# Performance work log

Hardware: AMD Instinct MI355X
Metric: run time of the kernel (lower is better)

## Reference

```python
import jax, jax.numpy as jnp
import numpy as np

B, L, D, H = 2, 2048, 1024, 16
DK = D // H  # head_dim = 64


def setup_inputs() -> dict:
    key = jax.random.key(0)
    ks = jax.random.split(key, 12)
    init = lambda k, shape, fan_in: jax.random.uniform(k, shape, jnp.float32, -1.0, 1.0) / np.sqrt(fan_in)
    inp = {
        "query": jax.random.normal(ks[0], (B, L, D), jnp.float32),
        "key": jax.random.normal(ks[1], (B, L, D), jnp.float32),
        "value": jax.random.normal(ks[2], (B, L, D), jnp.float32),
        # causal mask [B, 1, L, L], True = attend
        "mask": jnp.broadcast_to(jnp.tril(jnp.ones((L, L), bool))[None, None], (B, 1, L, L)),
        "wq": init(ks[3], (D, D), D), "bq": jnp.zeros((D,), jnp.float32),
        "wk": init(ks[4], (D, D), D), "bk": jnp.zeros((D,), jnp.float32),
        "wv": init(ks[5], (D, D), D), "bv": jnp.zeros((D,), jnp.float32),
        "wo": init(ks[6], (D, D), D), "bo": jnp.zeros((D,), jnp.float32),
    }
    return inp


def reference(query, key, value, mask, wq, bq, wk, bk, wv, bv, wo, bo):
    b, l, d = query.shape
    split = lambda x: x.reshape(b, l, H, DK).transpose(0, 2, 1, 3)  # B H L dk
    Q = split(query @ wq + bq)
    K = split(key @ wk + bk)
    V = split(value @ wv + bv)
    scores = jnp.einsum("bhqd,bhkd->bhqk", Q, K) / jnp.sqrt(jnp.float32(DK))
    probs = jax.nn.softmax(scores, axis=-1, where=mask)  # masked-out rows contribute 0
    attn = jnp.einsum("bhqk,bhkd->bhqd", probs, V)
    out = attn.transpose(0, 2, 1, 3).reshape(b, l, d)  # B L D
    return out @ wo + bo
```

## Files before the change

### kernel.cpp

```cpp
#include <hip/hip_runtime.h>
#include <hip/hip_bf16.h>

typedef __bf16 bf16x8 __attribute__((ext_vector_type(8)));
typedef __bf16 bf16x4 __attribute__((ext_vector_type(4)));
typedef float floatx4 __attribute__((ext_vector_type(4)));

constexpr int Bn  = 2;
constexpr int Ln  = 2048;
constexpr int Dn  = 1024;
constexpr int Hn  = 16;
constexpr int DKn = 64;
constexpr int Mn  = Bn * Ln;

__device__ __forceinline__ void gload_lds16(const void* g, void* l) {
  __builtin_amdgcn_global_load_lds(
      (const __attribute__((address_space(1))) void*)g,
      (__attribute__((address_space(3))) void*)l, 16, 0, 0);
}

__global__ __launch_bounds__(256) void cvt3(
    const float* __restrict__ q, const float* __restrict__ k,
    const float* __restrict__ v, __hip_bfloat16* __restrict__ dst)
{
  const float* src = blockIdx.z == 0 ? q : blockIdx.z == 1 ? k : v;
  __hip_bfloat16* d = dst + (size_t)blockIdx.z * Mn * Dn;
  const int i = blockIdx.x * 256 + threadIdx.x;
  const float4 a = ((const float4*)src)[i * 2];
  const float4 b = ((const float4*)src)[i * 2 + 1];
  bf16x8 o;
  o[0] = (__bf16)a.x; o[1] = (__bf16)a.y; o[2] = (__bf16)a.z; o[3] = (__bf16)a.w;
  o[4] = (__bf16)b.x; o[5] = (__bf16)b.y; o[6] = (__bf16)b.z; o[7] = (__bf16)b.w;
  ((bf16x8*)d)[i] = o;
}

__global__ __launch_bounds__(256) void transpose4(
    const float* __restrict__ wq, const float* __restrict__ wk,
    const float* __restrict__ wv, const float* __restrict__ wo,
    __hip_bfloat16* __restrict__ out)
{
  const float* src = blockIdx.z == 0 ? wq : blockIdx.z == 1 ? wk
                   : blockIdx.z == 2 ? wv : wo;
  __hip_bfloat16* dst = out + (size_t)blockIdx.z * Dn * Dn;
  __shared__ __bf16 tile[32][33];
  const int tx = threadIdx.x, ty = threadIdx.y;
  const int x = blockIdx.x * 32 + tx;
  const int y = blockIdx.y * 32 + ty;
  for (int i = 0; i < 32; i += 8)
    tile[ty + i][tx] = (__bf16)src[(size_t)(y + i) * Dn + x];
  __syncthreads();
  const int x2 = blockIdx.y * 32 + tx;
  const int y2 = blockIdx.x * 32 + ty;
  for (int i = 0; i < 32; i += 8)
    ((__bf16*)dst)[(size_t)(y2 + i) * Dn + x2] = tile[tx][ty + i];
}

__global__ __launch_bounds__(256) void gemm_qkv(
    const __hip_bfloat16* __restrict__ Abf,
    const __hip_bfloat16* __restrict__ wT,
    const float* __restrict__ bq, const float* __restrict__ bk,
    const float* __restrict__ bv,
    __hip_bfloat16* __restrict__ Qp, __hip_bfloat16* __restrict__ Kp,
    __hip_bfloat16* __restrict__ Vt)
{
  constexpr int BK = 32;
  __shared__ __bf16 As[128][BK];
  __shared__ __bf16 Ws[128][BK];
  const int z = blockIdx.z;
  const __hip_bfloat16* A  = Abf + (size_t)z * Mn * Dn;
  const __hip_bfloat16* WT = wT  + (size_t)z * Dn * Dn;
  const float* bias = z == 0 ? bq : z == 1 ? bk : bv;

  const int m0 = blockIdx.x * 128;
  const int n0 = blockIdx.y * 128;
  const int tid  = threadIdx.x;
  const int lane = tid & 63;
  const int wave = tid >> 6;
  const int quad = lane >> 4;
  const int l16  = lane & 15;
  const int wm = (wave >> 1) * 64;
  const int wn = (wave & 1) * 64;
  const int srow = tid >> 2;
  const int scol = (tid & 3) * 8;

  floatx4 acc[4][4];
  for (int i = 0; i < 4; i++)
    for (int j = 0; j < 4; j++)
      acc[i][j] = (floatx4){0.f, 0.f, 0.f, 0.f};

  for (int k0 = 0; k0 < Dn; k0 += BK) {
    for (int half = 0; half < 2; half++) {
      gload_lds16(&A [(size_t)(m0 + srow + half * 64) * Dn + k0 + scol],
                  &As[srow + half * 64][scol]);
      gload_lds16(&WT[(size_t)(n0 + srow + half * 64) * Dn + k0 + scol],
                  &Ws[srow + half * 64][scol]);
    }
    __syncthreads();
    bf16x8 af[4], wf[4];
    for (int i = 0; i < 4; i++) af[i] = *(const bf16x8*)&As[wm + i * 16 + l16][quad * 8];
    for (int j = 0; j < 4; j++) wf[j] = *(const bf16x8*)&Ws[wn + j * 16 + l16][quad * 8];
    for (int i = 0; i < 4; i++)
      for (int j = 0; j < 4; j++)
        acc[i][j] = __builtin_amdgcn_mfma_f32_16x16x32_bf16(af[i], wf[j], acc[i][j], 0, 0, 0);
    __syncthreads();
  }

  if (z == 2) {
    for (int j = 0; j < 4; j++) {
      const int n = n0 + wn + j * 16 + l16;
      const float bvv = bias[n];
      const int h = n >> 6, dk = n & 63;
      for (int i = 0; i < 4; i++) {
        const int m = m0 + wm + i * 16 + quad * 4;
        const int b = m >> 11, li = m & (Ln - 1);
        bf16x4 pk;
        for (int r = 0; r < 4; r++) pk[r] = (__bf16)(acc[i][j][r] + bvv);
        *(bf16x4*)&Vt[(((size_t)(b * Hn + h)) * DKn + dk) * Ln + li] = pk;
      }
    }
  } else {
    __hip_bfloat16* out = z == 0 ? Qp : Kp;
    for (int j = 0; j < 4; j++) {
      const int n = n0 + wn + j * 16 + l16;
      const float bvv = bias[n];
      const int h = n >> 6, dk = n & 63;
      for (int i = 0; i < 4; i++) {
        for (int r = 0; r < 4; r++) {
          const int m = m0 + wm + i * 16 + quad * 4 + r;
          const int b = m >> 11, li = m & (Ln - 1);
          out[(((size_t)(b * Hn + h)) * Ln + li) * DKn + dk] =
              __float2bfloat16(acc[i][j][r] + bvv);
        }
      }
    }
  }
}

__global__ __launch_bounds__(256) void gemm_out(
    const __hip_bfloat16* __restrict__ A,
    const __hip_bfloat16* __restrict__ WT,
    const float* __restrict__ bias,
    float* __restrict__ out)
{
  constexpr int BK = 32;
  __shared__ __bf16 As[128][BK];
  __shared__ __bf16 Ws[64][BK];
  const int m0 = blockIdx.x * 128;
  const int n0 = blockIdx.y * 64;
  const int tid  = threadIdx.x;
  const int lane = tid & 63;
  const int wave = tid >> 6;
  const int quad = lane >> 4;
  const int l16  = lane & 15;
  const int wm = (wave >> 1) * 64;
  const int wn = (wave & 1) * 32;
  const int srow = tid >> 2;
  const int scol = (tid & 3) * 8;

  floatx4 acc[4][2];
  for (int i = 0; i < 4; i++)
    for (int j = 0; j < 2; j++)
      acc[i][j] = (floatx4){0.f, 0.f, 0.f, 0.f};

  for (int k0 = 0; k0 < Dn; k0 += BK) {
    for (int half = 0; half < 2; half++)
      gload_lds16(&A [(size_t)(m0 + srow + half * 64) * Dn + k0 + scol],
                  &As[srow + half * 64][scol]);
    gload_lds16(&WT[(size_t)(n0 + srow) * Dn + k0 + scol], &Ws[srow][scol]);
    __syncthreads();
    bf16x8 af[4], wf[2];
    for (int i = 0; i < 4; i++) af[i] = *(const bf16x8*)&As[wm + i * 16 + l16][quad * 8];
    for (int j = 0; j < 2; j++) wf[j] = *(const bf16x8*)&Ws[wn + j * 16 + l16][quad * 8];
    for (int i = 0; i < 4; i++)
      for (int j = 0; j < 2; j++)
        acc[i][j] = __builtin_amdgcn_mfma_f32_16x16x32_bf16(af[i], wf[j], acc[i][j], 0, 0, 0);
    __syncthreads();
  }

  for (int j = 0; j < 2; j++) {
    const int n = n0 + wn + j * 16 + l16;
    const float bvv = bias[n];
    for (int i = 0; i < 4; i++)
      for (int r = 0; r < 4; r++) {
        const int m = m0 + wm + i * 16 + quad * 4 + r;
        out[(size_t)m * Dn + n] = acc[i][j][r] + bvv;
      }
  }
}

__global__ __launch_bounds__(64) void attn_flash(
    const __hip_bfloat16* __restrict__ Qp,
    const __hip_bfloat16* __restrict__ Kp,
    const __hip_bfloat16* __restrict__ Vt,
    __hip_bfloat16* __restrict__ attn)
{
  const int bh   = blockIdx.x;
  const int qt   = (gridDim.y - 1 - blockIdx.y);
  const int lane = threadIdx.x & 63;
  const int quad = lane >> 4;
  const int l16  = lane & 15;
  const int qb   = qt * 32;

  const __hip_bfloat16* Qh = Qp + (size_t)bh * Ln * DKn;
  const __hip_bfloat16* Kh = Kp + (size_t)bh * Ln * DKn;
  const __hip_bfloat16* Vh = Vt + (size_t)bh * DKn * Ln;

  __shared__ __align__(16) __bf16 Plds[2][16][72];

  bf16x8 qf[2][2];
  for (int m = 0; m < 2; m++)
    for (int dd = 0; dd < 2; dd++)
      qf[m][dd] = *(const bf16x8*)&Qh[(size_t)(qb + m * 16 + l16) * DKn + dd * 32 + quad * 8];

  floatx4 o[2][4];
  for (int m = 0; m < 2; m++)
    for (int t = 0; t < 4; t++) o[m][t] = (floatx4){0.f, 0.f, 0.f, 0.f};
  float lp[2] = {0.f, 0.f};

  const int kend = qb + 32;
  for (int kt = 0; kt < kend; kt += 64) {
    floatx4 s[2][4];
    for (int m = 0; m < 2; m++)
      for (int sub = 0; sub < 4; sub++) s[m][sub] = (floatx4){0.f, 0.f, 0.f, 0.f};
    for (int sub = 0; sub < 4; sub++)
      for (int dd = 0; dd < 2; dd++) {
        bf16x8 kf = *(const bf16x8*)&Kh[(size_t)(kt + sub * 16 + l16) * DKn + dd * 32 + quad * 8];
        s[0][sub] = __builtin_amdgcn_mfma_f32_16x16x32_bf16(kf, qf[0][dd], s[0][sub], 0, 0, 0);
        s[1][sub] = __builtin_amdgcn_mfma_f32_16x16x32_bf16(kf, qf[1][dd], s[1][sub], 0, 0, 0);
      }

    bf16x8 vf[4][2];
    for (int t = 0; t < 4; t++)
      for (int kc = 0; kc < 2; kc++)
        vf[t][kc] = *(const bf16x8*)&Vh[(size_t)(t * 16 + l16) * Ln + kt + kc * 32 + quad * 8];

    for (int m = 0; m < 2; m++) {
      const bool needmask = (kt + 64 > qb + m * 16);
      const int qg = qb + m * 16 + l16;
      for (int sub = 0; sub < 4; sub++) {
        bf16x4 pk;
        for (int r = 0; r < 4; r++) {
          float sv = s[m][sub][r];
          if (needmask && (kt + sub * 16 + quad * 4 + r > qg)) sv = -1e30f;
          const float e = __builtin_exp2f(__builtin_fmaf(sv, 0.18033688f, -11.5415603f));
          lp[m] += e;
          pk[r] = (__bf16)e;
        }
        *(bf16x4*)&Plds[m][l16][sub * 16 + quad * 4] = pk;
      }
    }
    __asm__ volatile("s_waitcnt lgkmcnt(0)" ::: "memory");

    bf16x8 pf[2][2];
    for (int m = 0; m < 2; m++)
      for (int kc = 0; kc < 2; kc++)
        pf[m][kc] = *(const bf16x8*)&Plds[m][l16][kc * 32 + quad * 8];
    for (int m = 0; m < 2; m++)
      for (int t = 0; t < 4; t++)
        for (int kc = 0; kc < 2; kc++)
          o[m][t] = __builtin_amdgcn_mfma_f32_16x16x32_bf16(pf[m][kc], vf[t][kc], o[m][t], 0, 0, 0);
  }

  const int b = bh >> 4, h = bh & 15;
  for (int m = 0; m < 2; m++) {
    float lf = lp[m];
    lf += __shfl_xor(lf, 16);
    lf += __shfl_xor(lf, 32);
    for (int r = 0; r < 4; r++) {
      const float lr = __shfl(lf, (lane & 48) | (quad * 4 + r));
      const float inv = 1.0f / lr;
      const int ql = qb + m * 16 + quad * 4 + r;
      const size_t base = ((size_t)b * Ln + ql) * Dn + h * DKn;
      for (int t = 0; t < 4; t++)
        attn[base + t * 16 + l16] = __float2bfloat16(o[m][t][r] * inv);
    }
  }
}

extern "C" void kernel_launch(void* const* d_in, const int* in_sizes, int n_in,
                              void* d_out, int out_size, void* d_ws, size_t ws_size,
                              hipStream_t stream) {
  const float* query = (const float*)d_in[0];
  const float* key_  = (const float*)d_in[1];
  const float* value = (const float*)d_in[2];
  const float* wq = (const float*)d_in[4];
  const float* bq = (const float*)d_in[5];
  const float* wk = (const float*)d_in[6];
  const float* bk = (const float*)d_in[7];
  const float* wv = (const float*)d_in[8];
  const float* bv = (const float*)d_in[9];
  const float* wo = (const float*)d_in[10];
  const float* bo = (const float*)d_in[11];

  const size_t T   = (size_t)Mn * Dn;
  const size_t WSZ = (size_t)Dn * Dn;
  __hip_bfloat16* Abf  = (__hip_bfloat16*)d_ws;
  __hip_bfloat16* Qp   = Abf + 3 * T;
  __hip_bfloat16* Kp   = Qp + T;
  __hip_bfloat16* Vt   = Kp + T;
  __hip_bfloat16* wT   = Vt + T;
  __hip_bfloat16* attn = Abf;

  transpose4<<<dim3(Dn / 32, Dn / 32, 4), dim3(32, 8), 0, stream>>>(wq, wk, wv, wo, wT);
  cvt3<<<dim3((int)(T / 2048), 1, 3), 256, 0, stream>>>(query, key_, value, Abf);
  gemm_qkv<<<dim3(Mn / 128, Dn / 128, 3), 256, 0, stream>>>(Abf, wT, bq, bk, bv, Qp, Kp, Vt);
  attn_flash<<<dim3(Bn * Hn, Ln / 32), 64, 0, stream>>>(Qp, Kp, Vt, attn);
  gemm_out<<<dim3(Mn / 128, Dn / 64), 256, 0, stream>>>(attn, wT + 3 * WSZ, bo, (float*)d_out);
}
```

Baseline: 284.7 us.

## Share K/V tiles across four waves via double-buffered LDS in attention

The attention kernel now runs four waves per block, each owning 32 query rows. The waves share K and V tiles that are loaded asynchronously into swizzled, double-buffered LDS, replacing the per-wave global loads. Separately, the Q/K projection GEMM swaps its MFMA operands so each lane holds four consecutive head-dim values, which lets it store packed bf16x4 values with a vectorized bias load. The trade-offs are block-level syncs, waves that idle on tiles past their causal end, and coarser work granularity.

```diff
diff --git a/kernel.cpp b/kernel.cpp
--- a/kernel.cpp
+++ b/kernel.cpp
@@ -98,9 +98,15 @@
     bf16x8 af[4], wf[4];
     for (int i = 0; i < 4; i++) af[i] = *(const bf16x8*)&As[wm + i * 16 + l16][quad * 8];
     for (int j = 0; j < 4; j++) wf[j] = *(const bf16x8*)&Ws[wn + j * 16 + l16][quad * 8];
-    for (int i = 0; i < 4; i++)
-      for (int j = 0; j < 4; j++)
-        acc[i][j] = __builtin_amdgcn_mfma_f32_16x16x32_bf16(af[i], wf[j], acc[i][j], 0, 0, 0);
+    if (z == 2) {
+      for (int i = 0; i < 4; i++)
+        for (int j = 0; j < 4; j++)
+          acc[i][j] = __builtin_amdgcn_mfma_f32_16x16x32_bf16(af[i], wf[j], acc[i][j], 0, 0, 0);
+    } else {
+      for (int i = 0; i < 4; i++)
+        for (int j = 0; j < 4; j++)
+          acc[i][j] = __builtin_amdgcn_mfma_f32_16x16x32_bf16(wf[j], af[i], acc[i][j], 0, 0, 0);
+    }
     __syncthreads();
   }
 
@@ -120,16 +126,18 @@
   } else {
     __hip_bfloat16* out = z == 0 ? Qp : Kp;
     for (int j = 0; j < 4; j++) {
-      const int n = n0 + wn + j * 16 + l16;
-      const float bvv = bias[n];
-      const int h = n >> 6, dk = n & 63;
+      const int nq = n0 + wn + j * 16 + quad * 4;
+      const float4 b4 = *(const float4*)&bias[nq];
+      const int h = nq >> 6, dk = nq & 63;
       for (int i = 0; i < 4; i++) {
-        for (int r = 0; r < 4; r++) {
-          const int m = m0 + wm + i * 16 + quad * 4 + r;
-          const int b = m >> 11, li = m & (Ln - 1);
-          out[(((size_t)(b * Hn + h)) * Ln + li) * DKn + dk] =
-              __float2bfloat16(acc[i][j][r] + bvv);
-        }
+        const int m = m0 + wm + i * 16 + l16;
+        const int b = m >> 11, li = m & (Ln - 1);
+        bf16x4 pk;
+        pk[0] = (__bf16)(acc[i][j][0] + b4.x);
+        pk[1] = (__bf16)(acc[i][j][1] + b4.y);
+        pk[2] = (__bf16)(acc[i][j][2] + b4.z);
+        pk[3] = (__bf16)(acc[i][j][3] + b4.w);
+        *(bf16x4*)&out[(((size_t)(b * Hn + h)) * Ln + li) * DKn + dk] = pk;
       }
     }
   }
@@ -187,7 +195,7 @@
   }
 }
 
-__global__ __launch_bounds__(64) void attn_flash(
+__global__ __launch_bounds__(256) void attn_flash(
     const __hip_bfloat16* __restrict__ Qp,
     const __hip_bfloat16* __restrict__ Kp,
     const __hip_bfloat16* __restrict__ Vt,
@@ -195,69 +203,94 @@
 {
   const int bh   = blockIdx.x;
   const int qt   = (gridDim.y - 1 - blockIdx.y);
-  const int lane = threadIdx.x & 63;
+  const int tid  = threadIdx.x;
+  const int wave = tid >> 6;
+  const int lane = tid & 63;
   const int quad = lane >> 4;
   const int l16  = lane & 15;
-  const int qb   = qt * 32;
+  const int qb0  = qt * 128;
+  const int qw   = qb0 + wave * 32;
 
   const __hip_bfloat16* Qh = Qp + (size_t)bh * Ln * DKn;
   const __hip_bfloat16* Kh = Kp + (size_t)bh * Ln * DKn;
   const __hip_bfloat16* Vh = Vt + (size_t)bh * DKn * Ln;
 
-  __shared__ __align__(16) __bf16 Plds[2][16][72];
+  __shared__ __align__(16) __bf16 Ks[2][64][64];
+  __shared__ __align__(16) __bf16 Vs[2][64][64];
+  __shared__ __align__(16) __bf16 Plds[4][2][16][72];
 
   bf16x8 qf[2][2];
   for (int m = 0; m < 2; m++)
     for (int dd = 0; dd < 2; dd++)
-      qf[m][dd] = *(const bf16x8*)&Qh[(size_t)(qb + m * 16 + l16) * DKn + dd * 32 + quad * 8];
+      qf[m][dd] = *(const bf16x8*)&Qh[(size_t)(qw + m * 16 + l16) * DKn + dd * 32 + quad * 8];
 
   floatx4 o[2][4];
   for (int m = 0; m < 2; m++)
     for (int t = 0; t < 4; t++) o[m][t] = (floatx4){0.f, 0.f, 0.f, 0.f};
   float lp[2] = {0.f, 0.f};
 
-  const int kend = qb + 32;
-  for (int kt = 0; kt < kend; kt += 64) {
-    floatx4 s[2][4];
-    for (int m = 0; m < 2; m++)
-      for (int sub = 0; sub < 4; sub++) s[m][sub] = (floatx4){0.f, 0.f, 0.f, 0.f};
-    for (int sub = 0; sub < 4; sub++)
-      for (int dd = 0; dd < 2; dd++) {
-        bf16x8 kf = *(const bf16x8*)&Kh[(size_t)(kt + sub * 16 + l16) * DKn + dd * 32 + quad * 8];
-        s[0][sub] = __builtin_amdgcn_mfma_f32_16x16x32_bf16(kf, qf[0][dd], s[0][sub], 0, 0, 0);
-        s[1][sub] = __builtin_amdgcn_mfma_f32_16x16x32_bf16(kf, qf[1][dd], s[1][sub], 0, 0, 0);
-      }
-
-    bf16x8 vf[4][2];
-    for (int t = 0; t < 4; t++)
-      for (int kc = 0; kc < 2; kc++)
-        vf[t][kc] = *(const bf16x8*)&Vh[(size_t)(t * 16 + l16) * Ln + kt + kc * 32 + quad * 8];
-
-    for (int m = 0; m < 2; m++) {
-      const bool needmask = (kt + 64 > qb + m * 16);
-      const int qg = qb + m * 16 + l16;
-      for (int sub = 0; sub < 4; sub++) {
-        bf16x4 pk;
-        for (int r = 0; r < 4; r++) {
-          float sv = s[m][sub][r];
-          if (needmask && (kt + sub * 16 + quad * 4 + r > qg)) sv = -1e30f;
-          const float e = __builtin_exp2f(__builtin_fmaf(sv, 0.18033688f, -11.5415603f));
-          lp[m] += e;
-          pk[r] = (__bf16)e;
+  const int srow8 = lane >> 3;
+  const int gch   = (lane & 7) ^ srow8;
+  const int xs    = (l16 & 7);
+
+  auto stage = [&](int buf, int kt) {
+    for (int s = 0; s < 2; s++) {
+      const int u = wave + s * 4;
+      gload_lds16(Kh + (size_t)(kt + u * 8 + srow8) * DKn + gch * 8,
+                  &Ks[buf][u * 8][0] + (size_t)lane * 8);
+      gload_lds16(Vh + (size_t)(u * 8 + srow8) * Ln + kt + gch * 8,
+                  &Vs[buf][u * 8][0] + (size_t)lane * 8);
+    }
+  };
+
+  const int kend_w = qw + 32;
+  const int kend_b = qb0 + 128;
+  stage(0, 0);
+  int buf = 0;
+  for (int kt = 0; kt < kend_b; kt += 64, buf ^= 1) {
+    __syncthreads();
+    if (kt + 64 < kend_b) stage(buf ^ 1, kt + 64);
+    if (kt < kend_w) {
+      floatx4 s[2][4];
+      for (int m = 0; m < 2; m++)
+        for (int sub = 0; sub < 4; sub++) s[m][sub] = (floatx4){0.f, 0.f, 0.f, 0.f};
+      for (int sub = 0; sub < 4; sub++)
+        for (int dd = 0; dd < 2; dd++) {
+          bf16x8 kf = *(const bf16x8*)&Ks[buf][sub * 16 + l16][((dd * 4 + quad) ^ xs) * 8];
+          s[0][sub] = __builtin_amdgcn_mfma_f32_16x16x32_bf16(kf, qf[0][dd], s[0][sub], 0, 0, 0);
+          s[1][sub] = __builtin_amdgcn_mfma_f32_16x16x32_bf16(kf, qf[1][dd], s[1][sub], 0, 0, 0);
         }
-        *(bf16x4*)&Plds[m][l16][sub * 16 + quad * 4] = pk;
-      }
-    }
-    __asm__ volatile("s_waitcnt lgkmcnt(0)" ::: "memory");
-
-    bf16x8 pf[2][2];
-    for (int m = 0; m < 2; m++)
-      for (int kc = 0; kc < 2; kc++)
-        pf[m][kc] = *(const bf16x8*)&Plds[m][l16][kc * 32 + quad * 8];
-    for (int m = 0; m < 2; m++)
+      bf16x8 vf[4][2];
       for (int t = 0; t < 4; t++)
         for (int kc = 0; kc < 2; kc++)
-          o[m][t] = __builtin_amdgcn_mfma_f32_16x16x32_bf16(pf[m][kc], vf[t][kc], o[m][t], 0, 0, 0);
+          vf[t][kc] = *(const bf16x8*)&Vs[buf][t * 16 + l16][((kc * 4 + quad) ^ xs) * 8];
+
+      for (int m = 0; m < 2; m++) {
+        const bool needmask = (kt + 64 > qw + m * 16);
+        const int qg = qw + m * 16 + l16;
+        for (int sub = 0; sub < 4; sub++) {
+          bf16x4 pk;
+          for (int r = 0; r < 4; r++) {
+            float sv = s[m][sub][r];
+            if (needmask && (kt + sub * 16 + quad * 4 + r > qg)) sv = -1e30f;
+            const float e = __builtin_exp2f(__builtin_fmaf(sv, 0.18033688f, -11.5415603f));
+            lp[m] += e;
+            pk[r] = (__bf16)e;
+          }
+          *(bf16x4*)&Plds[wave][m][l16][sub * 16 + quad * 4] = pk;
+        }
+      }
+      __asm__ volatile("s_waitcnt lgkmcnt(0)" ::: "memory");
+
+      bf16x8 pf[2][2];
+      for (int m = 0; m < 2; m++)
+        for (int kc = 0; kc < 2; kc++)
+          pf[m][kc] = *(const bf16x8*)&Plds[wave][m][l16][kc * 32 + quad * 8];
+      for (int m = 0; m < 2; m++)
+        for (int t = 0; t < 4; t++)
+          for (int kc = 0; kc < 2; kc++)
+            o[m][t] = __builtin_amdgcn_mfma_f32_16x16x32_bf16(pf[m][kc], vf[t][kc], o[m][t], 0, 0, 0);
+    }
   }
 
   const int b = bh >> 4, h = bh & 15;
@@ -268,7 +301,7 @@
     for (int r = 0; r < 4; r++) {
       const float lr = __shfl(lf, (lane & 48) | (quad * 4 + r));
       const float inv = 1.0f / lr;
-      const int ql = qb + m * 16 + quad * 4 + r;
+      const int ql = qw + m * 16 + quad * 4 + r;
       const size_t base = ((size_t)b * Ln + ql) * Dn + h * DKn;
       for (int t = 0; t < 4; t++)
         attn[base + t * 16 + l16] = __float2bfloat16(o[m][t][r] * inv);
@@ -303,6 +336,6 @@
   transpose4<<<dim3(Dn / 32, Dn / 32, 4), dim3(32, 8), 0, stream>>>(wq, wk, wv, wo, wT);
   cvt3<<<dim3((int)(T / 2048), 1, 3), 256, 0, stream>>>(query, key_, value, Abf);
   gemm_qkv<<<dim3(Mn / 128, Dn / 128, 3), 256, 0, stream>>>(Abf, wT, bq, bk, bv, Qp, Kp, Vt);
-  attn_flash<<<dim3(Bn * Hn, Ln / 32), 64, 0, stream>>>(Qp, Kp, Vt, attn);
+  attn_flash<<<dim3(Bn * Hn, Ln / 128), 256, 0, stream>>>(Qp, Kp, Vt, attn);
   gemm_out<<<dim3(Mn / 128, Dn / 64), 256, 0, stream>>>(attn, wT + 3 * WSZ, bo, (float*)d_out);
 }
```

Result: faster. 271.8 us (-4.5%).
